# Kernel tuning notes

Hardware: AMD Instinct MI355X
Metric: run time of the kernel (lower is better)

Reference implementation:

```python
import jax, jax.numpy as jnp
import numpy as np

B, S, D, H = 2, 2048, 1024, 16
HD = D // H  # head dim = 64


def setup_inputs() -> dict:
    key = jax.random.key(0)
    k0, k1, k2 = jax.random.split(key, 3)
    x = jax.random.normal(k0, (B, S, D), dtype=jnp.float32)
    # fused QKV projection: nn.Linear(D, 3D) -> weight [3D, D], bias [3D]
    Wqkv_w = jax.random.normal(k1, (3 * D, D), dtype=jnp.float32) * (1.0 / np.sqrt(D))
    Wqkv_b = jnp.zeros((3 * D,), dtype=jnp.float32)
    out_w = jax.random.normal(k2, (D, D), dtype=jnp.float32) * (1.0 / np.sqrt(D))
    out_b = jnp.zeros((D,), dtype=jnp.float32)
    # ALiBi-like additive bias, shape [1, H, 1, S] (broadcasts over queries)
    slopes = 2.0 ** (-8.0 * jnp.arange(1, H + 1, dtype=jnp.float32) / H)  # [H]
    dist = (S - 1) - jnp.arange(S, dtype=jnp.float32)                      # [S]
    attn_bias = (-slopes[:, None] * dist[None, :]).reshape(1, H, 1, S)
    # key padding mask: second sequence is padded by 256 tokens at the end
    lengths = jnp.array([S, S - 256])
    attention_mask = jnp.arange(S)[None, :] < lengths[:, None]             # [B, S] bool
    return {"x": x, "Wqkv_w": Wqkv_w, "Wqkv_b": Wqkv_b, "out_w": out_w,
            "out_b": out_b, "attn_bias": attn_bias, "attention_mask": attention_mask}


def reference(x, Wqkv_w, Wqkv_b, out_w, out_b, attn_bias, attention_mask):
    b, s, d = x.shape
    # fused QKV projection, then chunk into q, k, v along feature dim
    qkv = jnp.einsum('bsd,ed->bse', x, Wqkv_w) + Wqkv_b  # [b, s, 3d]
    q, k, v = jnp.split(qkv, 3, axis=-1)
    # b s (h hd) -> b h s hd
    q = q.reshape(b, s, H, HD).transpose(0, 2, 1, 3)
    k = k.reshape(b, s, H, HD).transpose(0, 2, 1, 3)
    v = v.reshape(b, s, H, HD).transpose(0, 2, 1, 3)
    softmax_scale = 1.0 / np.sqrt(HD)
    aw = jnp.einsum('bhqe,bhke->bhqk', q, k) * softmax_scale  # [b, H, s, s]
    aw = aw + attn_bias  # attn_bias broadcasts [1,H,1,s] -> [b,H,s,s]
    min_val = jnp.finfo(aw.dtype).min
    # key padding mask: mask positions where attention_mask is False
    aw = jnp.where(attention_mask[:, None, None, :], aw, min_val)
    # causal mask (is_causal=True, s_q == s_k)
    causal = jnp.tril(jnp.ones((s, s), dtype=bool))
    aw = jnp.where(causal[None, None, :, :], aw, min_val)
    p = jax.nn.softmax(aw, axis=-1)
    out = jnp.einsum('bhqk,bhke->bhqe', p, v)  # [b, H, s, HD]
    out = out.transpose(0, 2, 1, 3).reshape(b, s, d)
    return jnp.einsum('bsd,ed->bse', out, out_w) + out_b
```

## Files before the change

### kernel.cpp

```cpp
#include <hip/hip_runtime.h>
#include <hip/hip_bf16.h>
#include <stdint.h>

typedef __attribute__((ext_vector_type(8))) short s16x8;
typedef __attribute__((ext_vector_type(8))) unsigned short u16x8;
typedef __attribute__((ext_vector_type(4))) float f32x4;

#define SEQ 2048
#define LOG2E 1.44269504088896f

__device__ __forceinline__ unsigned short f2b(float x) {
  union { __hip_bfloat16 h; unsigned short u; } cv;
  cv.h = __float2bfloat16(x);
  return cv.u;
}

__device__ __forceinline__ float exp2fast(float x) {
  float r;
  asm("v_exp_f32 %0, %1" : "=v"(r) : "v"(x));
  return r;
}

__device__ __forceinline__ void gload16(const void* g, void* l) {
  __builtin_amdgcn_global_load_lds(
      (const __attribute__((address_space(1))) void*)g,
      (__attribute__((address_space(3))) void*)l, 16, 0, 0);
}

__global__ void cvt_all(const float* __restrict__ x, const float* __restrict__ wq,
                        const float* __restrict__ ow, const float* __restrict__ abias,
                        const void* __restrict__ maskp,
                        __hip_bfloat16* __restrict__ xb, __hip_bfloat16* __restrict__ wqb,
                        __hip_bfloat16* __restrict__ owb, float* __restrict__ biasm) {
  const int i = blockIdx.x * 256 + threadIdx.x;
  if (i >= 2097152) {
    const int j = i - 2097152;
    const int b = j >> 15, h = (j >> 11) & 15, kv = j & 2047;
    const int* mi = (const int*)maskp;
    const unsigned char* mb = (const unsigned char*)maskp;
    const bool int_fmt = (mi[0] == 0 || mi[0] == 1);
    const bool ok = int_fmt ? (mi[b * SEQ + kv] != 0) : (mb[b * SEQ + kv] != 0);
    biasm[j] = ok ? abias[h * SEQ + kv] * LOG2E : -1e30f;
    return;
  }
  const float* src;
  __hip_bfloat16* dst;
  int off;
  if (i < 1048576) { src = x; dst = xb; off = i; }
  else if (i < 1835008) { src = wq; dst = wqb; off = i - 1048576; }
  else { src = ow; dst = owb; off = i - 1835008; }
  float4 v = reinterpret_cast<const float4*>(src)[off];
  ushort4 o;
  o.x = f2b(v.x); o.y = f2b(v.y); o.z = f2b(v.z); o.w = f2b(v.w);
  reinterpret_cast<ushort4*>(dst)[off] = o;
}

template <int MODE, int BM>
__global__ __launch_bounds__(256) void gemm_bt(
    const __hip_bfloat16* __restrict__ A, const __hip_bfloat16* __restrict__ B,
    const float* __restrict__ bias, void* __restrict__ Cout,
    __hip_bfloat16* __restrict__ Vt, int M, int N, int K) {
  constexpr int MR = BM / 32;
  __shared__ __align__(16) __hip_bfloat16 As[BM * 32];
  __shared__ __align__(16) __hip_bfloat16 Bs[128 * 32];
  const int tid = threadIdx.x;
  const int lane = tid & 63;
  const int w = tid >> 6;
  const int wr = w >> 1, wc = w & 1;
  const int rowg = blockIdx.x * BM;
  const int colg = blockIdx.y * 128;
  const int lr = lane & 15;
  const int lk = (lane >> 4) * 8;
  f32x4 acc[MR][4];
#pragma unroll
  for (int m = 0; m < MR; ++m)
#pragma unroll
    for (int n = 0; n < 4; ++n) acc[m][n] = (f32x4){0.f, 0.f, 0.f, 0.f};
  for (int kt = 0; kt < K; kt += 32) {
#pragma unroll
    for (int r = 0; r < BM / 64; ++r) {
      const int idx = r * 256 + tid;
      gload16(A + (size_t)(rowg + (idx >> 2)) * K + kt + (idx & 3) * 8, As + idx * 8);
    }
#pragma unroll
    for (int r = 0; r < 2; ++r) {
      const int idx = r * 256 + tid;
      gload16(B + (size_t)(colg + (idx >> 2)) * K + kt + (idx & 3) * 8, Bs + idx * 8);
    }
    __syncthreads();
    s16x8 af[MR], bfr[4];
#pragma unroll
    for (int m = 0; m < MR; ++m)
      af[m] = *reinterpret_cast<const s16x8*>(As + (wr * (BM / 2) + m * 16 + lr) * 32 + lk);
#pragma unroll
    for (int n = 0; n < 4; ++n)
      bfr[n] = *reinterpret_cast<const s16x8*>(Bs + (wc * 64 + n * 16 + lr) * 32 + lk);
#pragma unroll
    for (int m = 0; m < MR; ++m)
#pragma unroll
      for (int n = 0; n < 4; ++n)
        acc[m][n] = __builtin_amdgcn_mfma_f32_16x16x32_bf16(af[m], bfr[n], acc[m][n], 0, 0, 0);
    __syncthreads();
  }
  const int r0l = (lane >> 4) * 4;
#pragma unroll
  for (int m = 0; m < MR; ++m) {
#pragma unroll
    for (int n = 0; n < 4; ++n) {
      const int col = colg + wc * 64 + n * 16 + lr;
      const int row0 = rowg + wr * (BM / 2) + m * 16 + r0l;
      const float bv = bias[col];
      if (MODE == 0) {
        __hip_bfloat16* qkb = (__hip_bfloat16*)Cout;
        if (col < 1024) {
#pragma unroll
          for (int j = 0; j < 4; ++j)
            qkb[(size_t)(row0 + j) * 2048 + col] = __float2bfloat16(acc[m][n][j] + bv);
        } else if (col < 2048) {
          const int dd = col & 63;
          const int base = col - dd;
#pragma unroll
          for (int j = 0; j < 4; ++j) {
            const int s = row0 + j;
            qkb[(size_t)s * 2048 + base + (dd ^ ((s & 7) << 3))] =
                __float2bfloat16(acc[m][n][j] + bv);
          }
        } else {
          const int c2 = col - 2048;
          const int dd = c2 & 63;
          const int bb = row0 >> 11;
          const int s0 = (row0 & 2047) ^ ((dd & 7) << 3);
          ushort4 pk;
          unsigned short* pp = (unsigned short*)&pk;
#pragma unroll
          for (int j = 0; j < 4; ++j) pp[j] = f2b(acc[m][n][j] + bv);
          *reinterpret_cast<ushort4*>(
              Vt + ((size_t)(bb * 16 + (c2 >> 6)) * 64 + dd) * 2048 + s0) = pk;
        }
      } else {
        float* o = (float*)Cout;
#pragma unroll
        for (int j = 0; j < 4; ++j)
          o[(size_t)(row0 + j) * N + col] = acc[m][n][j] + bv;
      }
    }
  }
}

__device__ __forceinline__ int swz(int row, int byteInRow) {
  return row * 128 + (byteInRow ^ ((row & 7) << 4));
}

__device__ __forceinline__ void attn_tile(
    const char* Ks, const char* Vs, char* pw, const float* bmb,
    s16x8 aq0, s16x8 aq1, int lane, int kv0, int q_abs, bool causal,
    float& m_r, float& l_r, f32x4* oa) {
  const int lr = lane & 15;
  const int g = lane >> 4;
  const int lkB = g * 16;
  const float SCALE2 = 0.125f * LOG2E;
  f32x4 sf[4];
#pragma unroll
  for (int n = 0; n < 4; ++n) {
    s16x8 ak0 = *reinterpret_cast<const s16x8*>(Ks + swz(n * 16 + lr, lkB));
    s16x8 ak1 = *reinterpret_cast<const s16x8*>(Ks + swz(n * 16 + lr, 64 + lkB));
    f32x4 z = (f32x4){0.f, 0.f, 0.f, 0.f};
    z = __builtin_amdgcn_mfma_f32_16x16x32_bf16(ak0, aq0, z, 0, 0, 0);
    z = __builtin_amdgcn_mfma_f32_16x16x32_bf16(ak1, aq1, z, 0, 0, 0);
    sf[n] = z;
  }
#pragma unroll
  for (int n = 0; n < 4; ++n) {
    f32x4 bv = *reinterpret_cast<const f32x4*>(bmb + kv0 + n * 16 + g * 4);
#pragma unroll
    for (int j = 0; j < 4; ++j) sf[n][j] = fmaf(sf[n][j], SCALE2, bv[j]);
  }
  if (causal) {
    const int kvb = kv0 + g * 4;
#pragma unroll
    for (int n = 0; n < 4; ++n)
#pragma unroll
      for (int j = 0; j < 4; ++j)
        if (kvb + n * 16 + j > q_abs) sf[n][j] = -1e30f;
  }
  float mx[4];
#pragma unroll
  for (int n = 0; n < 4; ++n)
    mx[n] = fmaxf(fmaxf(sf[n][0], sf[n][1]), fmaxf(sf[n][2], sf[n][3]));
  float tm = fmaxf(fmaxf(mx[0], mx[1]), fmaxf(mx[2], mx[3]));
  tm = fmaxf(tm, __shfl_xor(tm, 16));
  tm = fmaxf(tm, __shfl_xor(tm, 32));
  const float mn = fmaxf(m_r, tm);
  const float al = exp2fast(m_r - mn);
  m_r = mn;
  float ps[4];
#pragma unroll
  for (int n = 0; n < 4; ++n) {
#pragma unroll
    for (int j = 0; j < 4; ++j) sf[n][j] = exp2fast(sf[n][j] - mn);
    ps[n] = (sf[n][0] + sf[n][1]) + (sf[n][2] + sf[n][3]);
  }
  float rs = (ps[0] + ps[1]) + (ps[2] + ps[3]);
  rs += __shfl_xor(rs, 16);
  rs += __shfl_xor(rs, 32);
  l_r = l_r * al + rs;
  float alj[4];
#pragma unroll
  for (int j = 0; j < 4; ++j) alj[j] = __shfl(al, g * 4 + j);
#pragma unroll
  for (int d = 0; d < 4; ++d)
#pragma unroll
    for (int j = 0; j < 4; ++j) oa[d][j] *= alj[j];
#pragma unroll
  for (int n = 0; n < 4; ++n) {
    union { ushort4 u; uint2 v; } pk;
    pk.u.x = f2b(sf[n][0]); pk.u.y = f2b(sf[n][1]);
    pk.u.z = f2b(sf[n][2]); pk.u.w = f2b(sf[n][3]);
    *reinterpret_cast<uint2*>(pw + lr * 128 + ((n * 32 + g * 8) ^ ((lr & 7) << 4))) = pk.v;
  }
  s16x8 pa0 = *reinterpret_cast<const s16x8*>(pw + swz(lr, lkB));
  s16x8 pa1 = *reinterpret_cast<const s16x8*>(pw + swz(lr, 64 + lkB));
#pragma unroll
  for (int d = 0; d < 4; ++d) {
    s16x8 bv0 = *reinterpret_cast<const s16x8*>(Vs + swz(d * 16 + lr, lkB));
    s16x8 bv1 = *reinterpret_cast<const s16x8*>(Vs + swz(d * 16 + lr, 64 + lkB));
    oa[d] = __builtin_amdgcn_mfma_f32_16x16x32_bf16(pa0, bv0, oa[d], 0, 0, 0);
    oa[d] = __builtin_amdgcn_mfma_f32_16x16x32_bf16(pa1, bv1, oa[d], 0, 0, 0);
  }
}

__global__ __launch_bounds__(512) void attn_fwd6(
    const __hip_bfloat16* __restrict__ qk, const __hip_bfloat16* __restrict__ Vt,
    const float* __restrict__ biasm, __hip_bfloat16* __restrict__ O) {
  __shared__ __align__(16) char KV[2][2][2][8192];
  __shared__ __align__(16) char Ps[8][2048];
  const int tid = threadIdx.x;
  const int lane = tid & 63;
  const int w = tid >> 6;
  const int wsub = w & 3;
  const int z = w >> 2;
  const int bid = blockIdx.x;
  const int qt = 31 - (bid >> 5);
  const int bh = bid & 31;
  const int b = bh >> 4, h = bh & 15;
  const int row0 = qt * 64 + wsub * 16;
  const int lr = lane & 15;
  const int g = lane >> 4;
  const int NTit = (qt >> 1) + 1;
  const __hip_bfloat16* qptr =
      qk + (size_t)(b * SEQ + row0 + lr) * 2048 + h * 64 + g * 8;
  const s16x8 aq0 = *reinterpret_cast<const s16x8*>(qptr);
  const s16x8 aq1 = *reinterpret_cast<const s16x8*>(qptr + 32);
  const int q_abs = row0 + lr;
  const float* bmb = biasm + (size_t)bh * 2048;
  float m_r = -INFINITY, l_r = 0.f;
  f32x4 oa[4];
#pragma unroll
  for (int d = 0; d < 4; ++d) oa[d] = (f32x4){0.f, 0.f, 0.f, 0.f};
  const int r_ = tid >> 3;
  const int c16 = tid & 7;
  const __hip_bfloat16* kb = qk + ((size_t)b * SEQ + r_) * 2048 + 1024 + h * 64 + c16 * 8;
  const __hip_bfloat16* vb = Vt + ((size_t)bh * 64 + r_) * 2048 + c16 * 8;
#define ISSUE(T, C)                                                     \
  {                                                                     \
    const int tE_ = 2 * (T);                                            \
    const int tO_ = (2 * (T) + 1 <= qt) ? (2 * (T) + 1) : qt;           \
    gload16(kb + (size_t)(tE_ * 64) * 2048, KV[0][C][0] + tid * 16);    \
    gload16(kb + (size_t)(tO_ * 64) * 2048, KV[1][C][0] + tid * 16);    \
    gload16(vb + tE_ * 64, KV[0][C][1] + tid * 16);                     \
    gload16(vb + tO_ * 64, KV[1][C][1] + tid * 16);                     \
  }
  ISSUE(0, 0);
  __syncthreads();
  int cur = 0;
  for (int t = 0; t < NTit; ++t) {
    if (t + 1 < NTit) ISSUE(t + 1, cur ^ 1);
    const int tz = 2 * t + z;
    if (tz <= qt)
      attn_tile(KV[z][cur][0], KV[z][cur][1], Ps[w], bmb, aq0, aq1, lane,
                tz * 64, q_abs, tz == qt, m_r, l_r, oa);
    __syncthreads();
    cur ^= 1;
  }
#undef ISSUE
  float* mlbuf = (float*)&KV[0][0][0][0];
  if (z == 1) {
    float* mo = (float*)(&Ps[0][0] + wsub * 4096);
#pragma unroll
    for (int d = 0; d < 4; ++d)
#pragma unroll
      for (int j = 0; j < 4; ++j)
        mo[(g * 4 + j) * 64 + d * 16 + lr] = oa[d][j];
    if (lane < 16) {
      mlbuf[wsub * 32 + lr] = m_r;
      mlbuf[wsub * 32 + 16 + lr] = l_r;
    }
  }
  __syncthreads();
  if (z == 0) {
    const float mB = mlbuf[wsub * 32 + lr];
    const float lB = mlbuf[wsub * 32 + 16 + lr];
    const float mS = fmaxf(m_r, mB);
    const float fA = exp2fast(m_r - mS);
    const float fB = exp2fast(mB - mS);
    const float linv = 1.0f / (l_r * fA + lB * fB);
    float fAj[4], fBj[4], lij[4];
#pragma unroll
    for (int j = 0; j < 4; ++j) {
      fAj[j] = __shfl(fA, g * 4 + j);
      fBj[j] = __shfl(fB, g * 4 + j);
      lij[j] = __shfl(linv, g * 4 + j);
    }
    const float* mo = (const float*)(&Ps[0][0] + wsub * 4096);
#pragma unroll
    for (int d = 0; d < 4; ++d)
#pragma unroll
      for (int j = 0; j < 4; ++j) {
        const float v =
            (oa[d][j] * fAj[j] + mo[(g * 4 + j) * 64 + d * 16 + lr] * fBj[j]) * lij[j];
        O[(size_t)(b * SEQ + row0 + g * 4 + j) * 1024 + h * 64 + d * 16 + lr] =
            __float2bfloat16(v);
      }
  }
}

extern "C" void kernel_launch(void* const* d_in, const int* in_sizes, int n_in,
                              void* d_out, int out_size, void* d_ws, size_t ws_size,
                              hipStream_t stream) {
  const float* x     = (const float*)d_in[0];
  const float* wqkv  = (const float*)d_in[1];
  const float* bqkv  = (const float*)d_in[2];
  const float* wout  = (const float*)d_in[3];
  const float* bout  = (const float*)d_in[4];
  const float* abias = (const float*)d_in[5];
  const void*  mask  = d_in[6];

  __hip_bfloat16* ws  = (__hip_bfloat16*)d_ws;
  __hip_bfloat16* xb  = ws;
  __hip_bfloat16* wqb = ws + 4194304;
  __hip_bfloat16* owb = ws + 7340032;
  __hip_bfloat16* qkb = ws + 8388608;
  __hip_bfloat16* vtb = ws + 16777216;
  float*          bmf = (float*)(ws + 20971520);
  __hip_bfloat16* aob = xb;

  cvt_all<<<8448, 256, 0, stream>>>(x, wqkv, wout, abias, mask, xb, wqb, owb, bmf);
  gemm_bt<0, 128><<<dim3(32, 24), 256, 0, stream>>>(xb, wqb, bqkv, (void*)qkb, vtb,
                                                    4096, 3072, 1024);
  attn_fwd6<<<1024, 512, 0, stream>>>(qkb, vtb, bmf, aob);
  gemm_bt<1, 64><<<dim3(64, 8), 256, 0, stream>>>(aob, owb, bout, d_out,
                                                  (__hip_bfloat16*)nullptr, 4096, 1024, 1024);
}
```

Measured before the change: 121.5 us.

## Hoist swizzle offsets, skip rescale conditionally, add MFMA priority and occupancy hint

Precomputes the swizzled LDS read and write offsets once per thread instead of per tile. Bias loads are issued before the QK MFMAs, and s_setprio raises wave priority around the MFMA blocks. A lazy-rescale rule skips the online-softmax max update and the output rescale unless some row's max grows by more than 8 in log2 units. The launch bounds gain a minimum of 4 blocks per CU, which may constrain registers. The lazy rescale keeps the exact result but lets exponentials reach up to 2^8 before normalisation, a small risk for bf16 P precision.

Result: no change. 121.3 us (-0.2%).

```diff
diff --git a/kernel.cpp b/kernel.cpp
--- a/kernel.cpp
+++ b/kernel.cpp
@@ -147,34 +147,33 @@
   }
 }
 
-__device__ __forceinline__ int swz(int row, int byteInRow) {
-  return row * 128 + (byteInRow ^ ((row & 7) << 4));
-}
-
 __device__ __forceinline__ void attn_tile(
     const char* Ks, const char* Vs, char* pw, const float* bmb,
     s16x8 aq0, s16x8 aq1, int lane, int kv0, int q_abs, bool causal,
+    int rd0, int rd1, const int* pwo,
     float& m_r, float& l_r, f32x4* oa) {
-  const int lr = lane & 15;
   const int g = lane >> 4;
-  const int lkB = g * 16;
   const float SCALE2 = 0.125f * LOG2E;
+  f32x4 bvp[4];
+#pragma unroll
+  for (int n = 0; n < 4; ++n)
+    bvp[n] = *reinterpret_cast<const f32x4*>(bmb + kv0 + n * 16 + g * 4);
   f32x4 sf[4];
+  __builtin_amdgcn_s_setprio(1);
 #pragma unroll
   for (int n = 0; n < 4; ++n) {
-    s16x8 ak0 = *reinterpret_cast<const s16x8*>(Ks + swz(n * 16 + lr, lkB));
-    s16x8 ak1 = *reinterpret_cast<const s16x8*>(Ks + swz(n * 16 + lr, 64 + lkB));
+    s16x8 ak0 = *reinterpret_cast<const s16x8*>(Ks + rd0 + n * 2048);
+    s16x8 ak1 = *reinterpret_cast<const s16x8*>(Ks + rd1 + n * 2048);
     f32x4 z = (f32x4){0.f, 0.f, 0.f, 0.f};
     z = __builtin_amdgcn_mfma_f32_16x16x32_bf16(ak0, aq0, z, 0, 0, 0);
     z = __builtin_amdgcn_mfma_f32_16x16x32_bf16(ak1, aq1, z, 0, 0, 0);
     sf[n] = z;
   }
-#pragma unroll
-  for (int n = 0; n < 4; ++n) {
-    f32x4 bv = *reinterpret_cast<const f32x4*>(bmb + kv0 + n * 16 + g * 4);
-#pragma unroll
-    for (int j = 0; j < 4; ++j) sf[n][j] = fmaf(sf[n][j], SCALE2, bv[j]);
-  }
+  __builtin_amdgcn_s_setprio(0);
+#pragma unroll
+  for (int n = 0; n < 4; ++n)
+#pragma unroll
+    for (int j = 0; j < 4; ++j) sf[n][j] = fmaf(sf[n][j], SCALE2, bvp[n][j]);
   if (causal) {
     const int kvb = kv0 + g * 4;
 #pragma unroll
@@ -190,46 +189,51 @@
   float tm = fmaxf(fmaxf(mx[0], mx[1]), fmaxf(mx[2], mx[3]));
   tm = fmaxf(tm, __shfl_xor(tm, 16));
   tm = fmaxf(tm, __shfl_xor(tm, 32));
-  const float mn = fmaxf(m_r, tm);
-  const float al = exp2fast(m_r - mn);
-  m_r = mn;
+  if (!__all(tm <= m_r + 8.0f)) {
+    const float mn = fmaxf(m_r, tm);
+    const float al = exp2fast(m_r - mn);
+    m_r = mn;
+    float alj[4];
+#pragma unroll
+    for (int j = 0; j < 4; ++j) alj[j] = __shfl(al, g * 4 + j);
+#pragma unroll
+    for (int d = 0; d < 4; ++d)
+#pragma unroll
+      for (int j = 0; j < 4; ++j) oa[d][j] *= alj[j];
+    l_r *= al;
+  }
   float ps[4];
 #pragma unroll
   for (int n = 0; n < 4; ++n) {
 #pragma unroll
-    for (int j = 0; j < 4; ++j) sf[n][j] = exp2fast(sf[n][j] - mn);
+    for (int j = 0; j < 4; ++j) sf[n][j] = exp2fast(sf[n][j] - m_r);
     ps[n] = (sf[n][0] + sf[n][1]) + (sf[n][2] + sf[n][3]);
   }
   float rs = (ps[0] + ps[1]) + (ps[2] + ps[3]);
   rs += __shfl_xor(rs, 16);
   rs += __shfl_xor(rs, 32);
-  l_r = l_r * al + rs;
-  float alj[4];
-#pragma unroll
-  for (int j = 0; j < 4; ++j) alj[j] = __shfl(al, g * 4 + j);
-#pragma unroll
-  for (int d = 0; d < 4; ++d)
-#pragma unroll
-    for (int j = 0; j < 4; ++j) oa[d][j] *= alj[j];
+  l_r += rs;
 #pragma unroll
   for (int n = 0; n < 4; ++n) {
     union { ushort4 u; uint2 v; } pk;
     pk.u.x = f2b(sf[n][0]); pk.u.y = f2b(sf[n][1]);
     pk.u.z = f2b(sf[n][2]); pk.u.w = f2b(sf[n][3]);
-    *reinterpret_cast<uint2*>(pw + lr * 128 + ((n * 32 + g * 8) ^ ((lr & 7) << 4))) = pk.v;
-  }
-  s16x8 pa0 = *reinterpret_cast<const s16x8*>(pw + swz(lr, lkB));
-  s16x8 pa1 = *reinterpret_cast<const s16x8*>(pw + swz(lr, 64 + lkB));
+    *reinterpret_cast<uint2*>(pw + pwo[n]) = pk.v;
+  }
+  s16x8 pa0 = *reinterpret_cast<const s16x8*>(pw + rd0);
+  s16x8 pa1 = *reinterpret_cast<const s16x8*>(pw + rd1);
+  __builtin_amdgcn_s_setprio(1);
 #pragma unroll
   for (int d = 0; d < 4; ++d) {
-    s16x8 bv0 = *reinterpret_cast<const s16x8*>(Vs + swz(d * 16 + lr, lkB));
-    s16x8 bv1 = *reinterpret_cast<const s16x8*>(Vs + swz(d * 16 + lr, 64 + lkB));
+    s16x8 bv0 = *reinterpret_cast<const s16x8*>(Vs + rd0 + d * 2048);
+    s16x8 bv1 = *reinterpret_cast<const s16x8*>(Vs + rd1 + d * 2048);
     oa[d] = __builtin_amdgcn_mfma_f32_16x16x32_bf16(pa0, bv0, oa[d], 0, 0, 0);
     oa[d] = __builtin_amdgcn_mfma_f32_16x16x32_bf16(pa1, bv1, oa[d], 0, 0, 0);
   }
-}
-
-__global__ __launch_bounds__(512) void attn_fwd6(
+  __builtin_amdgcn_s_setprio(0);
+}
+
+__global__ __launch_bounds__(512, 4) void attn_fwd6(
     const __hip_bfloat16* __restrict__ qk, const __hip_bfloat16* __restrict__ Vt,
     const float* __restrict__ biasm, __hip_bfloat16* __restrict__ O) {
   __shared__ __align__(16) char KV[2][2][2][8192];
@@ -247,6 +251,12 @@
   const int lr = lane & 15;
   const int g = lane >> 4;
   const int NTit = (qt >> 1) + 1;
+  const int xm = (lr & 7) << 4;
+  const int lkB = g * 16;
+  const int rd0 = lr * 128 + (lkB ^ xm);
+  const int rd1 = lr * 128 + ((64 + lkB) ^ xm);
+  const int pwo[4] = {lr * 128 + ((g * 8) ^ xm),       lr * 128 + ((32 + g * 8) ^ xm),
+                      lr * 128 + ((64 + g * 8) ^ xm),  lr * 128 + ((96 + g * 8) ^ xm)};
   const __hip_bfloat16* qptr =
       qk + (size_t)(b * SEQ + row0 + lr) * 2048 + h * 64 + g * 8;
   const s16x8 aq0 = *reinterpret_cast<const s16x8*>(qptr);
@@ -278,7 +288,7 @@
     const int tz = 2 * t + z;
     if (tz <= qt)
       attn_tile(KV[z][cur][0], KV[z][cur][1], Ps[w], bmb, aq0, aq1, lane,
-                tz * 64, q_abs, tz == qt, m_r, l_r, oa);
+                tz * 64, q_abs, tz == qt, rd0, rd1, pwo, m_r, l_r, oa);
     __syncthreads();
     cur ^= 1;
   }
```
